# Optimization experiments

Hardware: AMD Instinct MI355X
Metric: run time of the kernel (lower is better)

## Reference

```python
import jax, jax.numpy as jnp
import numpy as np

NEG = -1000000000.0  # matches torch masked_fill value


def setup_inputs() -> dict:
    key = jax.random.key(0)
    ks = jax.random.split(key, 9)
    B, L, E = 2, 2048, 1024
    s = 0.02
    return {
        "query": jax.random.normal(ks[0], (B, L, E), dtype=jnp.float32),
        "w_q_w": jax.random.normal(ks[1], (E, E), dtype=jnp.float32) * s,
        "w_q_b": jax.random.normal(ks[2], (E,), dtype=jnp.float32) * s,
        "w_k_w": jax.random.normal(ks[3], (E, E), dtype=jnp.float32) * s,
        "w_k_b": jax.random.normal(ks[4], (E,), dtype=jnp.float32) * s,
        "w_v_w": jax.random.normal(ks[5], (E, E), dtype=jnp.float32) * s,
        "w_v_b": jax.random.normal(ks[6], (E,), dtype=jnp.float32) * s,
        "w_o_w": jax.random.normal(ks[7], (E, E), dtype=jnp.float32) * s,
        "w_o_b": jax.random.normal(ks[8], (E,), dtype=jnp.float32) * s,
    }


def reference(query, w_q_w, w_q_b, w_k_w, w_k_b, w_v_w, w_v_b, w_o_w, w_o_b):
    # self-attention: key = value = query (forward passes None for key/value)
    B, L, E = query.shape
    H = 16
    d_k = E // H
    scale = 1.0 / jnp.sqrt(jnp.float32(d_k))

    def proj(x, w, b):
        # torch Linear: x @ w.T + b ; then split heads -> [B, H, L, d_k]
        return (x @ w.T + b).reshape(B, L, H, d_k).transpose(0, 2, 1, 3)

    Q = proj(query, w_q_w, w_q_b)
    K = proj(query, w_k_w, w_k_b)
    V = proj(query, w_v_w, w_v_b)

    # full L x S score matrix, as in the eager original
    scores = jnp.einsum('bhqd,bhkd->bhqk', Q, K) * scale
    # causal attn_bias: upper triangle filled with -1e9 (is_causal=True path)
    causal = jnp.tril(jnp.ones((L, L), dtype=bool))
    scores = scores + jnp.where(causal, 0.0, NEG).astype(scores.dtype)
    # softmax, clear_nan (nan -> 0), + 1e-12 epsilon; dropout_p = 0.0 (no-op)
    attn = jnp.nan_to_num(jax.nn.softmax(scores, axis=-1), nan=0.0) + 1e-12

    ctx = jnp.einsum('bhqk,bhkd->bhqd', attn, V)  # [B,H,L,d_k]
    ctx = ctx.transpose(0, 2, 1, 3).reshape(B, L, E)
    return ctx @ w_o_w.T + w_o_b
```

## Files before the change

### kernel.cpp

```cpp
#include <hip/hip_runtime.h>
#include <hip/hip_bf16.h>
#include <math.h>

typedef __bf16 bf16;
typedef __bf16 bf16x4 __attribute__((ext_vector_type(4)));
typedef __bf16 bf16x8 __attribute__((ext_vector_type(8)));
typedef float  f32x4  __attribute__((ext_vector_type(4)));
typedef float  float4v __attribute__((ext_vector_type(4)));
typedef unsigned short u16x4 __attribute__((ext_vector_type(4)));

#define MFMA(a,b,c) __builtin_amdgcn_mfma_f32_16x16x32_bf16((a),(b),(c),0,0,0)

#define QSCALE 0.18033688011112042f
#define EXP2(x) __builtin_amdgcn_exp2f(x)

__device__ __forceinline__ void gload16(const bf16* g, bf16* l) {
  __builtin_amdgcn_global_load_lds(
      (const __attribute__((address_space(1))) void*)g,
      (__attribute__((address_space(3))) void*)l, 16, 0, 0);
}

__device__ __forceinline__ int detect_f32(const unsigned short* __restrict__ p) {
  int bad = 0;
  #pragma unroll
  for (int j = 0; j < 32; ++j) {
    const float x = __uint_as_float(((unsigned)p[j]) << 16);
    bad |= !(fabsf(x) <= 0.5f);
  }
  return bad;
}

__global__ void cvt_all_kernel(const void* x, const void* wq, const void* wk,
                               const void* wv, const void* wo,
                               const void* bq, const void* bk, const void* bv,
                               const void* bo,
                               bf16* cX, bf16* cWq, bf16* cWk, bf16* cWv,
                               bf16* cWo, bf16* cB)
{
  const int isf = detect_f32((const unsigned short*)bq);
  const int NX = 1048576, NW = 262144, NB = 256;
  const int total = NX + 4 * NW + 4 * NB;
  for (int gid = blockIdx.x * blockDim.x + threadIdx.x; gid < total;
       gid += gridDim.x * blockDim.x) {
    const void* s; bf16* d; int off;
    if (gid < NX)                { s = x;  d = cX;  off = gid; }
    else if (gid < NX + NW)      { s = wq; d = cWq; off = gid - NX; }
    else if (gid < NX + 2 * NW)  { s = wk; d = cWk; off = gid - NX - NW; }
    else if (gid < NX + 3 * NW)  { s = wv; d = cWv; off = gid - NX - 2 * NW; }
    else if (gid < NX + 4 * NW)  { s = wo; d = cWo; off = gid - NX - 3 * NW; }
    else {
      const int r = gid - NX - 4 * NW;
      const int wb = r / NB; off = r % NB;
      s = (wb == 0) ? bq : (wb == 1) ? bk : (wb == 2) ? bv : bo;
      d = cB + wb * 1024;
    }
    float4v v;
    if (isf) v = ((const float4v*)s)[off];
    else {
      u16x4 u = ((const u16x4*)s)[off];
      v = (float4v){__uint_as_float((unsigned)u.x << 16),
                    __uint_as_float((unsigned)u.y << 16),
                    __uint_as_float((unsigned)u.z << 16),
                    __uint_as_float((unsigned)u.w << 16)};
    }
    bf16x4 ov = {(bf16)v.x, (bf16)v.y, (bf16)v.z, (bf16)v.w};
    *(bf16x4*)&d[off * 4] = ov;
  }
}

static __device__ __forceinline__ void gemm128_core(
    const bf16* __restrict__ X, const bf16* __restrict__ W,
    int bm, int bn, f32x4 acc[4][4])
{
  __shared__ __align__(16) bf16 Als[128][64];
  __shared__ __align__(16) bf16 Bls[128][64];
  const int t    = threadIdx.x;
  const int lane = t & 63;
  const int w    = t >> 6;
  const int wr   = w >> 1, wc = w & 1;
  const int fr   = lane & 15;
  const int fq   = lane >> 4;
  const int lrow = lane >> 3;
  const int sc   = ((((lane & 7) << 4) ^ (lrow << 4)) >> 1);
  const int X7   = (fr & 7) << 4;
  const char* Ab = (const char*)Als;
  const char* Bb = (const char*)Bls;

  #pragma unroll
  for (int m = 0; m < 4; ++m)
    #pragma unroll
    for (int n = 0; n < 4; ++n)
      acc[m][n] = (f32x4){0.f, 0.f, 0.f, 0.f};

  for (int k0 = 0; k0 < 1024; k0 += 64) {
    __syncthreads();
    #pragma unroll
    for (int p = 0; p < 4; ++p) {
      const int rb = p * 32 + w * 8;
      gload16(&X[(size_t)(bm + rb + lrow) * 1024 + k0 + sc], &Als[rb][0]);
      gload16(&W[(size_t)(bn + rb + lrow) * 1024 + k0 + sc], &Bls[rb][0]);
    }
    __syncthreads();
    #pragma unroll
    for (int kk = 0; kk < 64; kk += 32) {
      const int coff = (kk * 2 + fq * 16) ^ X7;
      bf16x8 a[4], b[4];
      #pragma unroll
      for (int m = 0; m < 4; ++m)
        a[m] = *(const bf16x8*)(Ab + (wr * 64 + m * 16 + fr) * 128 + coff);
      #pragma unroll
      for (int n = 0; n < 4; ++n)
        b[n] = *(const bf16x8*)(Bb + (wc * 64 + n * 16 + fr) * 128 + coff);
      __builtin_amdgcn_s_setprio(1);
      #pragma unroll
      for (int m = 0; m < 4; ++m)
        #pragma unroll
        for (int n = 0; n < 4; ++n)
          acc[m][n] = MFMA(a[m], b[n], acc[m][n]);
      __builtin_amdgcn_s_setprio(0);
    }
  }
}

__global__ __launch_bounds__(256, 3) void qkv_kernel(
    const bf16* __restrict__ X,
    const bf16* __restrict__ Wq, const bf16* __restrict__ Wk,
    const bf16* __restrict__ Wv, const bf16* __restrict__ Bias,
    bf16* __restrict__ Qo, bf16* __restrict__ Ko, bf16* __restrict__ Vto)
{
  const bf16 *W, *bias;
  bf16 *out;
  const int z = blockIdx.z;
  if (z == 0)      { W = Wq; bias = Bias;        out = Qo;  }
  else if (z == 1) { W = Wk; bias = Bias + 1024; out = Ko;  }
  else             { W = Wv; bias = Bias + 2048; out = Vto; }

  const int bm = blockIdx.x * 128, bn = blockIdx.y * 128;
  f32x4 acc[4][4];
  gemm128_core(X, W, bm, bn, acc);

  const int t = threadIdx.x, lane = t & 63, w = t >> 6;
  const int wr = w >> 1, wc = w & 1;
  const int fr = lane & 15, fq = lane >> 4;
  const float qs = (z == 0) ? QSCALE : 1.0f;

  #pragma unroll
  for (int n = 0; n < 4; ++n) {
    const int col = bn + wc * 64 + n * 16 + fr;
    const float bb = (float)bias[col];
    const int h = col >> 6, d = col & 63;
    if (z != 2) {
      #pragma unroll
      for (int m = 0; m < 4; ++m)
        #pragma unroll
        for (int r = 0; r < 4; ++r) {
          const int row = bm + wr * 64 + m * 16 + fq * 4 + r;
          const int b = row >> 11, li = row & 2047;
          out[(size_t)((b * 16 + h) * 2048 + li) * 64 + d] =
              (bf16)((acc[m][n][r] + bb) * qs);
        }
    } else {
      #pragma unroll
      for (int m = 0; m < 4; ++m) {
        const int tok0 = bm + wr * 64 + m * 16 + fq * 4;
        const int b = tok0 >> 11, li0 = tok0 & 2047;
        bf16x4 pk = {(bf16)(acc[m][n][0] + bb), (bf16)(acc[m][n][1] + bb),
                     (bf16)(acc[m][n][2] + bb), (bf16)(acc[m][n][3] + bb)};
        *(bf16x4*)&out[(size_t)((b * 16 + h) * 64 + d) * 2048 + li0] = pk;
      }
    }
  }
}

__global__ __launch_bounds__(256, 4) void attn_kernel(
    const bf16* __restrict__ Q, const bf16* __restrict__ K,
    const bf16* __restrict__ Vt, bf16* __restrict__ CTX)
{
  const int bx = (int)blockIdx.x;
  const int gen = bx >> 8;
  const int u = bx & 255;
  const int bh = u >> 3;
  const int j = u & 7;
  int qt;
  if (gen == 0)      qt = 31 - j;
  else if (gen == 1) qt = 16 + j;
  else if (gen == 2) qt = 15 - j;
  else               qt = j;

  const int t = threadIdx.x, lane = t & 63, w = t >> 6;
  const int fr = lane & 15, fq = lane >> 4;
  const bf16* Qb = Q  + (size_t)bh * 2048 * 64;
  const bf16* Kb = K  + (size_t)bh * 2048 * 64;
  const bf16* Vb = Vt + (size_t)bh * 64 * 2048;
  const int q0 = qt * 64 + w * 16;
  const int myq = q0 + fr;
  const int nt = qt + 1;

  __shared__ __align__(16) bf16 Kls[2][64][64];
  __shared__ __align__(16) bf16 Vls[2][64][64];
  __shared__ __align__(16) bf16 Pls[4][16][64];

  const int X7   = (fr & 7) << 4;
  const int off0 = fr * 128 + ((fq * 16) ^ X7);
  const int off1 = fr * 128 + ((64 + fq * 16) ^ X7);
  const char* Kb0 = (const char*)Kls;
  const char* Vb0 = (const char*)Vls;
  char* Pw = (char*)Pls + w * 2048 + fr * 128;
  int pwoff[4];
  #pragma unroll
  for (int g = 0; g < 4; ++g) pwoff[g] = ((g * 32 + fq * 8) ^ X7);
  const int proff0 = ((fq * 16) ^ X7);
  const int proff1 = ((64 + fq * 16) ^ X7);

  const int r8 = lane >> 3;
  const int cb = (lane & 7) << 4;
  const int sc = (cb ^ (r8 << 4)) >> 1;
  const bf16* gk0 = Kb + (size_t)(w * 8 + r8) * 64 + sc;
  const bf16* gk1 = Kb + (size_t)(32 + w * 8 + r8) * 64 + sc;
  const bf16* gv0 = Vb + (size_t)(w * 8 + r8) * 2048 + sc;
  const bf16* gv1 = Vb + (size_t)(32 + w * 8 + r8) * 2048 + sc;

  const bf16x8 qf0 = *(const bf16x8*)&Qb[(size_t)(q0 + fr) * 64 + fq * 8];
  const bf16x8 qf1 = *(const bf16x8*)&Qb[(size_t)(q0 + fr) * 64 + 32 + fq * 8];

  f32x4 o[4];
  #pragma unroll
  for (int g = 0; g < 4; ++g) o[g] = (f32x4){0.f, 0.f, 0.f, 0.f};
  float s_part = 0.f;

  gload16(gk0, &Kls[0][w * 8][0]);
  gload16(gk1, &Kls[0][32 + w * 8][0]);
  gload16(gv0, &Vls[0][w * 8][0]);
  gload16(gv1, &Vls[0][32 + w * 8][0]);
  gk0 += 4096; gk1 += 4096; gv0 += 64; gv1 += 64;
  __syncthreads();
  int cur = 0;

  for (int kt = 0; kt < nt; ++kt) {
    if (kt + 1 < nt) {
      bf16 (*Kn)[64] = Kls[cur ^ 1];
      bf16 (*Vn)[64] = Vls[cur ^ 1];
      gload16(gk0, &Kn[w * 8][0]);
      gload16(gk1, &Kn[32 + w * 8][0]);
      gload16(gv0, &Vn[w * 8][0]);
      gload16(gv1, &Vn[32 + w * 8][0]);
      gk0 += 4096; gk1 += 4096; gv0 += 64; gv1 += 64;
    }

    const char* kb = Kb0 + (cur << 13);
    const char* vb = Vb0 + (cur << 13);

    f32x4 S[4];
    __builtin_amdgcn_s_setprio(1);
    #pragma unroll
    for (int g = 0; g < 4; ++g) {
      bf16x8 kf0 = *(const bf16x8*)(kb + off0 + g * 2048);
      bf16x8 kf1 = *(const bf16x8*)(kb + off1 + g * 2048);
      f32x4 s = (f32x4){0.f, 0.f, 0.f, 0.f};
      s = MFMA(kf0, qf0, s);
      s = MFMA(kf1, qf1, s);
      S[g] = s;
    }
    __builtin_amdgcn_s_setprio(0);

    if (kt == qt) {
      #pragma unroll
      for (int g = 0; g < 4; ++g)
        #pragma unroll
        for (int r = 0; r < 4; ++r)
          S[g][r] = (kt * 64 + g * 16 + fq * 4 + r <= myq) ? S[g][r] : -1e9f;
    }
    #pragma unroll
    for (int g = 0; g < 4; ++g)
      #pragma unroll
      for (int r = 0; r < 4; ++r) {
        const float p = EXP2(S[g][r]);
        S[g][r] = p;
        s_part += p;
      }
    #pragma unroll
    for (int g = 0; g < 4; ++g) {
      bf16x4 pk = {(bf16)S[g][0], (bf16)S[g][1], (bf16)S[g][2], (bf16)S[g][3]};
      *(bf16x4*)(Pw + pwoff[g]) = pk;
    }
    __builtin_amdgcn_s_setprio(1);
    {
      bf16x8 pa0 = *(const bf16x8*)(Pw + proff0);
      #pragma unroll
      for (int g2 = 0; g2 < 4; ++g2) {
        bf16x8 vf = *(const bf16x8*)(vb + off0 + g2 * 2048);
        o[g2] = MFMA(pa0, vf, o[g2]);
      }
      bf16x8 pa1 = *(const bf16x8*)(Pw + proff1);
      #pragma unroll
      for (int g2 = 0; g2 < 4; ++g2) {
        bf16x8 vf = *(const bf16x8*)(vb + off1 + g2 * 2048);
        o[g2] = MFMA(pa1, vf, o[g2]);
      }
    }
    __builtin_amdgcn_s_setprio(0);
    __syncthreads();
    cur ^= 1;
  }

  float s_r = s_part;
  s_r += __shfl_xor(s_r, 16);
  s_r += __shfl_xor(s_r, 32);
  const float inv = __builtin_amdgcn_rcpf(fmaxf(s_r, 1e-30f));
  float invr[4];
  #pragma unroll
  for (int r = 0; r < 4; ++r) invr[r] = __shfl(inv, fq * 4 + r, 64);
  const int b = bh >> 4, h = bh & 15;
  #pragma unroll
  for (int r = 0; r < 4; ++r) {
    const int tok = b * 2048 + q0 + fq * 4 + r;
    #pragma unroll
    for (int g2 = 0; g2 < 4; ++g2)
      CTX[(size_t)tok * 1024 + h * 64 + g2 * 16 + fr] =
          (bf16)(o[g2][r] * invr[r]);
  }
}

__global__ __launch_bounds__(256, 4) void out_kernel(
    const bf16* __restrict__ CTXi, const bf16* __restrict__ Wo,
    const bf16* __restrict__ bo, void* __restrict__ Y,
    const unsigned short* __restrict__ det)
{
  __shared__ __align__(16) bf16 Als[128][64];
  __shared__ __align__(16) bf16 Bls[64][64];
  const int isf = detect_f32(det);
  const int bm = blockIdx.x * 128, bn = blockIdx.y * 64;
  const int t = threadIdx.x, lane = t & 63, w = t >> 6;
  const int wr = w >> 1, wc = w & 1;
  const int fr = lane & 15, fq = lane >> 4;
  const int lrow = lane >> 3;
  const int sc = ((((lane & 7) << 4) ^ (lrow << 4)) >> 1);
  const int X7 = (fr & 7) << 4;
  const char* Ab = (const char*)Als;
  const char* Bb = (const char*)Bls;

  f32x4 acc[4][2];
  #pragma unroll
  for (int m = 0; m < 4; ++m)
    #pragma unroll
    for (int n = 0; n < 2; ++n)
      acc[m][n] = (f32x4){0.f, 0.f, 0.f, 0.f};

  for (int k0 = 0; k0 < 1024; k0 += 64) {
    __syncthreads();
    #pragma unroll
    for (int p = 0; p < 4; ++p) {
      const int rb = p * 32 + w * 8;
      gload16(&CTXi[(size_t)(bm + rb + lrow) * 1024 + k0 + sc], &Als[rb][0]);
    }
    #pragma unroll
    for (int p = 0; p < 2; ++p) {
      const int rb = w * 16 + p * 8;
      gload16(&Wo[(size_t)(bn + rb + lrow) * 1024 + k0 + sc], &Bls[rb][0]);
    }
    __syncthreads();
    #pragma unroll
    for (int kk = 0; kk < 64; kk += 32) {
      const int coff = (kk * 2 + fq * 16) ^ X7;
      bf16x8 a[4], b[2];
      #pragma unroll
      for (int m = 0; m < 4; ++m)
        a[m] = *(const bf16x8*)(Ab + (wr * 64 + m * 16 + fr) * 128 + coff);
      #pragma unroll
      for (int n = 0; n < 2; ++n)
        b[n] = *(const bf16x8*)(Bb + (wc * 32 + n * 16 + fr) * 128 + coff);
      __builtin_amdgcn_s_setprio(1);
      #pragma unroll
      for (int m = 0; m < 4; ++m)
        #pragma unroll
        for (int n = 0; n < 2; ++n)
          acc[m][n] = MFMA(a[m], b[n], acc[m][n]);
      __builtin_amdgcn_s_setprio(0);
    }
  }

  #pragma unroll
  for (int n = 0; n < 2; ++n) {
    const int col = bn + wc * 32 + n * 16 + fr;
    const float bb = (float)bo[col];
    #pragma unroll
    for (int m = 0; m < 4; ++m)
      #pragma unroll
      for (int r = 0; r < 4; ++r) {
        const int row = bm + wr * 64 + m * 16 + fq * 4 + r;
        const size_t idx = (size_t)row * 1024 + col;
        const float v = acc[m][n][r] + bb;
        if (isf) ((float*)Y)[idx] = v;
        else     ((bf16*)Y)[idx] = (bf16)v;
      }
  }
}

extern "C" void kernel_launch(void* const* d_in, const int* in_sizes, int n_in,
                              void* d_out, int out_size, void* d_ws, size_t ws_size,
                              hipStream_t stream) {
  char* ws = (char*)d_ws;
  const size_t MB = 1024 * 1024;

  bf16* cX  = (bf16*)(ws + 1 * MB);
  bf16* cWq = (bf16*)(ws + 9 * MB);
  bf16* cWk = (bf16*)(ws + 11 * MB);
  bf16* cWv = (bf16*)(ws + 13 * MB);
  bf16* cWo = (bf16*)(ws + 15 * MB);
  bf16* cB  = (bf16*)(ws + 17 * MB);
  bf16* Qw  = (bf16*)(ws + 18 * MB);
  bf16* Kw  = (bf16*)(ws + 26 * MB);
  bf16* Vt  = (bf16*)(ws + 34 * MB);
  bf16* CT  = (bf16*)(ws + 42 * MB);

  cvt_all_kernel<<<2048, 256, 0, stream>>>(d_in[0], d_in[1], d_in[3], d_in[5],
                                           d_in[7], d_in[2], d_in[4], d_in[6],
                                           d_in[8], cX, cWq, cWk, cWv, cWo, cB);

  qkv_kernel<<<dim3(32, 8, 3), 256, 0, stream>>>(cX, cWq, cWk, cWv, cB,
                                                 Qw, Kw, Vt);
  attn_kernel<<<1024, 256, 0, stream>>>(Qw, Kw, Vt, CT);
  out_kernel<<<dim3(32, 16), 256, 0, stream>>>(CT, cWo, cB + 3072, d_out,
                                               (const unsigned short*)d_in[2]);
}
```

Measured before the change: 99.02 us.

## Double query tile per attention block to reuse K/V loads across 128 rows

Each attention block now handles 128 query rows (32 per wave, as two 16-row sub-tiles) instead of 64, halving the grid to 512 blocks. Each K/V tile loaded into LDS is reused by twice as many queries, and V fragments are loaded into registers once and shared by both sub-tiles. Waves skip key tiles entirely beyond their causal range. In exchange, register pressure rises (launch bounds relaxed to 2 blocks/CU), there are fewer blocks for load balancing, and waves inside a block become imbalanced near the diagonal.

Result: slower. 104.5 us (+5.5%).

```diff
diff --git a/kernel.cpp b/kernel.cpp
--- a/kernel.cpp
+++ b/kernel.cpp
@@ -172,7 +172,7 @@
   }
 }
 
-__global__ __launch_bounds__(256, 4) void attn_kernel(
+__global__ __launch_bounds__(256, 2) void attn_kernel(
     const bf16* __restrict__ Q, const bf16* __restrict__ K,
     const bf16* __restrict__ Vt, bf16* __restrict__ CTX)
 {
@@ -181,20 +181,17 @@
   const int u = bx & 255;
   const int bh = u >> 3;
   const int j = u & 7;
-  int qt;
-  if (gen == 0)      qt = 31 - j;
-  else if (gen == 1) qt = 16 + j;
-  else if (gen == 2) qt = 15 - j;
-  else               qt = j;
+  const int qt = gen ? j : 15 - j;
 
   const int t = threadIdx.x, lane = t & 63, w = t >> 6;
   const int fr = lane & 15, fq = lane >> 4;
   const bf16* Qb = Q  + (size_t)bh * 2048 * 64;
   const bf16* Kb = K  + (size_t)bh * 2048 * 64;
   const bf16* Vb = Vt + (size_t)bh * 64 * 2048;
-  const int q0 = qt * 64 + w * 16;
-  const int myq = q0 + fr;
-  const int nt = qt + 1;
+  const int q0w = qt * 128 + w * 32;
+  const int mqa = q0w + fr;
+  const int mqb = q0w + 16 + fr;
+  const int nt = 2 * qt + 2;
 
   __shared__ __align__(16) bf16 Kls[2][64][64];
   __shared__ __align__(16) bf16 Vls[2][64][64];
@@ -220,13 +217,18 @@
   const bf16* gv0 = Vb + (size_t)(w * 8 + r8) * 2048 + sc;
   const bf16* gv1 = Vb + (size_t)(32 + w * 8 + r8) * 2048 + sc;
 
-  const bf16x8 qf0 = *(const bf16x8*)&Qb[(size_t)(q0 + fr) * 64 + fq * 8];
-  const bf16x8 qf1 = *(const bf16x8*)&Qb[(size_t)(q0 + fr) * 64 + 32 + fq * 8];
-
-  f32x4 o[4];
-  #pragma unroll
-  for (int g = 0; g < 4; ++g) o[g] = (f32x4){0.f, 0.f, 0.f, 0.f};
-  float s_part = 0.f;
+  const bf16x8 qa0 = *(const bf16x8*)&Qb[(size_t)(q0w + fr) * 64 + fq * 8];
+  const bf16x8 qa1 = *(const bf16x8*)&Qb[(size_t)(q0w + fr) * 64 + 32 + fq * 8];
+  const bf16x8 qb0 = *(const bf16x8*)&Qb[(size_t)(q0w + 16 + fr) * 64 + fq * 8];
+  const bf16x8 qb1 = *(const bf16x8*)&Qb[(size_t)(q0w + 16 + fr) * 64 + 32 + fq * 8];
+
+  f32x4 oa[4], ob[4];
+  #pragma unroll
+  for (int g = 0; g < 4; ++g) {
+    oa[g] = (f32x4){0.f, 0.f, 0.f, 0.f};
+    ob[g] = (f32x4){0.f, 0.f, 0.f, 0.f};
+  }
+  float s_a = 0.f, s_b = 0.f;
 
   gload16(gk0, &Kls[0][w * 8][0]);
   gload16(gk1, &Kls[0][32 + w * 8][0]);
@@ -247,77 +249,115 @@
       gk0 += 4096; gk1 += 4096; gv0 += 64; gv1 += 64;
     }
 
-    const char* kb = Kb0 + (cur << 13);
-    const char* vb = Vb0 + (cur << 13);
-
-    f32x4 S[4];
-    __builtin_amdgcn_s_setprio(1);
-    #pragma unroll
-    for (int g = 0; g < 4; ++g) {
-      bf16x8 kf0 = *(const bf16x8*)(kb + off0 + g * 2048);
-      bf16x8 kf1 = *(const bf16x8*)(kb + off1 + g * 2048);
-      f32x4 s = (f32x4){0.f, 0.f, 0.f, 0.f};
-      s = MFMA(kf0, qf0, s);
-      s = MFMA(kf1, qf1, s);
-      S[g] = s;
-    }
-    __builtin_amdgcn_s_setprio(0);
-
-    if (kt == qt) {
+    const int kbase = kt * 64;
+    if (kbase <= q0w + 31) {
+      const char* kb = Kb0 + (cur << 13);
+      const char* vb = Vb0 + (cur << 13);
+
+      f32x4 Sa[4], Sb[4];
+      __builtin_amdgcn_s_setprio(1);
+      #pragma unroll
+      for (int g = 0; g < 4; ++g) {
+        bf16x8 kf0 = *(const bf16x8*)(kb + off0 + g * 2048);
+        bf16x8 kf1 = *(const bf16x8*)(kb + off1 + g * 2048);
+        f32x4 sa = (f32x4){0.f, 0.f, 0.f, 0.f};
+        sa = MFMA(kf0, qa0, sa);
+        sa = MFMA(kf1, qa1, sa);
+        Sa[g] = sa;
+        f32x4 sb = (f32x4){0.f, 0.f, 0.f, 0.f};
+        sb = MFMA(kf0, qb0, sb);
+        sb = MFMA(kf1, qb1, sb);
+        Sb[g] = sb;
+      }
+      __builtin_amdgcn_s_setprio(0);
+
+      if (kbase + 63 > q0w) {
+        #pragma unroll
+        for (int g = 0; g < 4; ++g)
+          #pragma unroll
+          for (int r = 0; r < 4; ++r) {
+            const int key = kbase + g * 16 + fq * 4 + r;
+            Sa[g][r] = (key <= mqa) ? Sa[g][r] : -1e9f;
+            Sb[g][r] = (key <= mqb) ? Sb[g][r] : -1e9f;
+          }
+      }
       #pragma unroll
       for (int g = 0; g < 4; ++g)
         #pragma unroll
-        for (int r = 0; r < 4; ++r)
-          S[g][r] = (kt * 64 + g * 16 + fq * 4 + r <= myq) ? S[g][r] : -1e9f;
-    }
-    #pragma unroll
-    for (int g = 0; g < 4; ++g)
-      #pragma unroll
-      for (int r = 0; r < 4; ++r) {
-        const float p = EXP2(S[g][r]);
-        S[g][r] = p;
-        s_part += p;
-      }
-    #pragma unroll
-    for (int g = 0; g < 4; ++g) {
-      bf16x4 pk = {(bf16)S[g][0], (bf16)S[g][1], (bf16)S[g][2], (bf16)S[g][3]};
-      *(bf16x4*)(Pw + pwoff[g]) = pk;
-    }
-    __builtin_amdgcn_s_setprio(1);
-    {
-      bf16x8 pa0 = *(const bf16x8*)(Pw + proff0);
+        for (int r = 0; r < 4; ++r) {
+          const float pa_ = EXP2(Sa[g][r]);
+          Sa[g][r] = pa_; s_a += pa_;
+          const float pb_ = EXP2(Sb[g][r]);
+          Sb[g][r] = pb_; s_b += pb_;
+        }
+      bf16x8 vf[8];
       #pragma unroll
       for (int g2 = 0; g2 < 4; ++g2) {
-        bf16x8 vf = *(const bf16x8*)(vb + off0 + g2 * 2048);
-        o[g2] = MFMA(pa0, vf, o[g2]);
-      }
-      bf16x8 pa1 = *(const bf16x8*)(Pw + proff1);
-      #pragma unroll
-      for (int g2 = 0; g2 < 4; ++g2) {
-        bf16x8 vf = *(const bf16x8*)(vb + off1 + g2 * 2048);
-        o[g2] = MFMA(pa1, vf, o[g2]);
-      }
-    }
-    __builtin_amdgcn_s_setprio(0);
+        vf[g2]     = *(const bf16x8*)(vb + off0 + g2 * 2048);
+        vf[4 + g2] = *(const bf16x8*)(vb + off1 + g2 * 2048);
+      }
+      #pragma unroll
+      for (int g = 0; g < 4; ++g) {
+        bf16x4 pk = {(bf16)Sa[g][0], (bf16)Sa[g][1], (bf16)Sa[g][2],
+                     (bf16)Sa[g][3]};
+        *(bf16x4*)(Pw + pwoff[g]) = pk;
+      }
+      {
+        bf16x8 pa0 = *(const bf16x8*)(Pw + proff0);
+        bf16x8 pa1 = *(const bf16x8*)(Pw + proff1);
+        __builtin_amdgcn_s_setprio(1);
+        #pragma unroll
+        for (int g2 = 0; g2 < 4; ++g2) {
+          oa[g2] = MFMA(pa0, vf[g2], oa[g2]);
+          oa[g2] = MFMA(pa1, vf[4 + g2], oa[g2]);
+        }
+        __builtin_amdgcn_s_setprio(0);
+      }
+      #pragma unroll
+      for (int g = 0; g < 4; ++g) {
+        bf16x4 pk = {(bf16)Sb[g][0], (bf16)Sb[g][1], (bf16)Sb[g][2],
+                     (bf16)Sb[g][3]};
+        *(bf16x4*)(Pw + pwoff[g]) = pk;
+      }
+      {
+        bf16x8 pb0 = *(const bf16x8*)(Pw + proff0);
+        bf16x8 pb1 = *(const bf16x8*)(Pw + proff1);
+        __builtin_amdgcn_s_setprio(1);
+        #pragma unroll
+        for (int g2 = 0; g2 < 4; ++g2) {
+          ob[g2] = MFMA(pb0, vf[g2], ob[g2]);
+          ob[g2] = MFMA(pb1, vf[4 + g2], ob[g2]);
+        }
+        __builtin_amdgcn_s_setprio(0);
+      }
+    }
     __syncthreads();
     cur ^= 1;
   }
 
-  float s_r = s_part;
-  s_r += __shfl_xor(s_r, 16);
-  s_r += __shfl_xor(s_r, 32);
-  const float inv = __builtin_amdgcn_rcpf(fmaxf(s_r, 1e-30f));
-  float invr[4];
-  #pragma unroll
-  for (int r = 0; r < 4; ++r) invr[r] = __shfl(inv, fq * 4 + r, 64);
+  float sra = s_a, srb = s_b;
+  sra += __shfl_xor(sra, 16); sra += __shfl_xor(sra, 32);
+  srb += __shfl_xor(srb, 16); srb += __shfl_xor(srb, 32);
+  const float inva = __builtin_amdgcn_rcpf(fmaxf(sra, 1e-30f));
+  const float invb = __builtin_amdgcn_rcpf(fmaxf(srb, 1e-30f));
+  float invar[4], invbr[4];
+  #pragma unroll
+  for (int r = 0; r < 4; ++r) {
+    invar[r] = __shfl(inva, fq * 4 + r, 64);
+    invbr[r] = __shfl(invb, fq * 4 + r, 64);
+  }
   const int b = bh >> 4, h = bh & 15;
   #pragma unroll
   for (int r = 0; r < 4; ++r) {
-    const int tok = b * 2048 + q0 + fq * 4 + r;
-    #pragma unroll
-    for (int g2 = 0; g2 < 4; ++g2)
-      CTX[(size_t)tok * 1024 + h * 64 + g2 * 16 + fr] =
-          (bf16)(o[g2][r] * invr[r]);
+    const int toka = b * 2048 + q0w + fq * 4 + r;
+    const int tokb = toka + 16;
+    #pragma unroll
+    for (int g2 = 0; g2 < 4; ++g2) {
+      CTX[(size_t)toka * 1024 + h * 64 + g2 * 16 + fr] =
+          (bf16)(oa[g2][r] * invar[r]);
+      CTX[(size_t)tokb * 1024 + h * 64 + g2 * 16 + fr] =
+          (bf16)(ob[g2][r] * invbr[r]);
+    }
   }
 }
 
@@ -419,7 +459,7 @@
 
   qkv_kernel<<<dim3(32, 8, 3), 256, 0, stream>>>(cX, cWq, cWk, cWv, cB,
                                                  Qw, Kw, Vt);
-  attn_kernel<<<1024, 256, 0, stream>>>(Qw, Kw, Vt, CT);
+  attn_kernel<<<512, 256, 0, stream>>>(Qw, Kw, Vt, CT);
   out_kernel<<<dim3(32, 16), 256, 0, stream>>>(CT, cWo, cB + 3072, d_out,
                                                (const unsigned short*)d_in[2]);
 }
```
